# Kernel tuning notes

Measured on AMD Instinct MI355X. Metric: run time of the kernel, lower is better.

The kernel has to match this reference:

```python
import jax, jax.numpy as jnp
import numpy as np

D = 256      # d_model
H = 8        # n_heads
HD = D // H  # head_dim = 32
P = 16       # point dim per head


def setup_inputs() -> dict:
    key = jax.random.key(0)
    ks = jax.random.split(key, 12)
    B, S = 2, 2048
    w = lambda k, shape: jax.random.normal(k, shape, jnp.float32) * 0.02
    return {
        "seq_repr": jax.random.normal(ks[0], (B, S, D), jnp.float32),
        "coords": jax.random.normal(ks[1], (B, S, 3, 3), jnp.float32),
        "frames": jax.random.normal(ks[2], (B, S, 4), jnp.float32),
        "mask": jnp.ones((B, S), jnp.int32),
        "Wq": w(ks[3], (D, D)), "bq": jnp.zeros((D,), jnp.float32),
        "Wk": w(ks[4], (D, D)), "bk": jnp.zeros((D,), jnp.float32),
        "Wv": w(ks[5], (D, D)), "bv": jnp.zeros((D,), jnp.float32),
        "Wpq": w(ks[6], (3, H * P)), "bpq": jnp.zeros((H * P,), jnp.float32),
        "Wpk": w(ks[7], (3, H * P)), "bpk": jnp.zeros((H * P,), jnp.float32),
        "Wo": w(ks[8], (D, D)), "bo": jnp.zeros((D,), jnp.float32),
        "Wpo": w(ks[9], (H * P, 3)), "bpo": jnp.zeros((3,), jnp.float32),
        "attn_bias": jnp.zeros((H,), jnp.float32),
    }


def reference(seq_repr, coords, frames, mask, Wq, bq, Wk, bk, Wv, bv,
              Wpq, bpq, Wpk, bpk, Wo, bo, Wpo, bpo, attn_bias):
    B, S, _ = seq_repr.shape
    q = (seq_repr @ Wq + bq).reshape(B, S, H, HD)
    k = (seq_repr @ Wk + bk).reshape(B, S, H, HD)
    v = (seq_repr @ Wv + bv).reshape(B, S, H, HD)

    rep = coords[..., 1, :]                                  # [B,S,3] representative atom
    pq = (rep @ Wpq + bpq).reshape(B, S, H, P)
    pk = (rep @ Wpk + bpk).reshape(B, S, H, P)

    scale = 1.0 / np.sqrt(HD)
    scores = (jnp.einsum('bihd,bjhd->bhij', q, k) * scale
              + jnp.einsum('bihp,bjhp->bhij', pq, pk) * 0.25  # 1/sqrt(16)
              + attn_bias[None, :, None, None])

    mask2d = (mask[:, :, None] * mask[:, None, :])[:, None]  # [B,1,S,S]
    scores = jnp.where(mask2d == 0, jnp.float32(-1e9), scores)

    w = jax.nn.softmax(scores, axis=-1)                      # [B,H,S,S]

    seq_ctx = jnp.einsum('bhij,bjhd->bihd', w, v).reshape(B, S, D)
    pt_ctx = jnp.einsum('bhij,bjhp->bihp', w, pq).reshape(B, S, H * P)

    seq_out = seq_ctx @ Wo + bo                              # [B,S,D]
    point_out = pt_ctx @ Wpo + bpo                           # [B,S,3]
    return (seq_out, point_out)
```

## Files before the change

### kernel.cpp

```cpp
#include <hip/hip_runtime.h>
#include <hip/hip_bf16.h>

#define D_ 256
#define H_ 8
#define B_ 2
#define S_ 2048
#define MTOT 4096
#define AUGQ 64
#define NBH 16
#define KPAD 72
#define NSPLIT 4
#define NJ 8
#define LOG2E 1.4426950408889634f

typedef __attribute__((ext_vector_type(8))) short short8;
typedef __attribute__((ext_vector_type(4))) short short4v;
typedef __attribute__((ext_vector_type(4))) float f32x4;

static __device__ __forceinline__ short bf16_of(float f) {
  union { __hip_bfloat16 h; short s; } u;
  u.h = __float2bfloat16(f);
  return u.s;
}
static __device__ __forceinline__ float f_of_bf16(short s) {
  union { float f; unsigned int u; } u;
  u.u = ((unsigned int)(unsigned short)s) << 16;
  return u.f;
}

static __device__ __forceinline__ int sinv64(int c) {
  return (((((c >> 2) & 1) << 1) | ((c >> 5) & 1)) << 4) + (((c >> 3) & 3) << 2) + (c & 3);
}


__global__ __launch_bounds__(256) void prep_all(
    const float* __restrict__ Wq, const float* __restrict__ Wk,
    const float* __restrict__ Wv, const float* __restrict__ Wo,
    const float* __restrict__ X, const float* __restrict__ coords,
    const int* __restrict__ mask,
    const float* __restrict__ Wpq, const float* __restrict__ bpq,
    const float* __restrict__ Wpk, const float* __restrict__ bpk,
    short* __restrict__ Wqkv_t, short* __restrict__ Wo_t,
    short* __restrict__ Xb,
    short* __restrict__ Qa, short* __restrict__ Ka, short* __restrict__ VaT) {
  int bid = blockIdx.x, tid = threadIdx.x;

  if (bid < 64) {
    __shared__ short T[64][72];
    const float* src;
    short* dst;
    int k0, n0g;
    if (bid < 48) {
      int nt = bid >> 2;
      k0 = (bid & 3) * 64;
      n0g = nt * 64;
      src = (n0g < 256) ? Wq : (n0g < 512 ? Wk : Wv);
      dst = Wqkv_t;
    } else {
      int t2 = bid - 48;
      k0 = (t2 & 3) * 64;
      n0g = (t2 >> 2) * 64;
      src = Wo;
      dst = Wo_t;
    }
    int ncol = n0g & 255;
    int rr = tid >> 4, cc = (tid & 15) * 4;
#pragma unroll
    for (int i = 0; i < 4; i++) {
      int r = rr + i * 16;
      f32x4 v = *reinterpret_cast<const f32x4*>(&src[(size_t)(k0 + r) * 256 + ncol + cc]);
      T[cc + 0][r] = bf16_of(v[0]);
      T[cc + 1][r] = bf16_of(v[1]);
      T[cc + 2][r] = bf16_of(v[2]);
      T[cc + 3][r] = bf16_of(v[3]);
    }
    __syncthreads();
    int n = tid >> 2, kk = (tid & 3) * 16;
    *reinterpret_cast<short8*>(&dst[(size_t)(n0g + n) * 256 + k0 + kk]) =
        *reinterpret_cast<const short8*>(&T[n][kk]);
    *reinterpret_cast<short8*>(&dst[(size_t)(n0g + n) * 256 + k0 + kk + 8]) =
        *reinterpret_cast<const short8*>(&T[n][kk + 8]);
    return;
  }

  if (bid < 576) {
    size_t i = (size_t)(bid - 64) * 2048 + tid * 8;
    f32x4 v0 = *reinterpret_cast<const f32x4*>(&X[i]);
    f32x4 v1 = *reinterpret_cast<const f32x4*>(&X[i + 4]);
    short8 o;
    o[0] = bf16_of(v0[0]); o[1] = bf16_of(v0[1]); o[2] = bf16_of(v0[2]); o[3] = bf16_of(v0[3]);
    o[4] = bf16_of(v1[0]); o[5] = bf16_of(v1[1]); o[6] = bf16_of(v1[2]); o[7] = bf16_of(v1[3]);
    *reinterpret_cast<short8*>(&Xb[i]) = o;
    return;
  }

  if (bid < 704) {
    int idx = (bid - 576) * 256 + tid;
    int m = idx >> 3, h = idx & 7;
    int b = m >> 11, s = m & 2047;
    float r0 = coords[m * 9 + 3], r1 = coords[m * 9 + 4], r2 = coords[m * 9 + 5];
    size_t base = ((size_t)(b * 8 + h) * S_ + s) * AUGQ;
    short8 pqv[2], pkv[2];
#pragma unroll
    for (int c = 0; c < 2; c++)
#pragma unroll
      for (int i = 0; i < 8; i++) {
        int j = h * 16 + c * 8 + i;
        float pq = r0 * Wpq[j] + r1 * Wpq[128 + j] + r2 * Wpq[256 + j] + bpq[j];
        float pk = r0 * Wpk[j] + r1 * Wpk[128 + j] + r2 * Wpk[256 + j] + bpk[j];
        pqv[c][i] = bf16_of(pq * LOG2E);
        pkv[c][i] = bf16_of(pk * 0.25f);
      }
    short8 padq = {};
    padq[0] = bf16_of(LOG2E);
    short8 padk = {};
    padk[0] = mask[m] ? (short)0 : bf16_of(-1e9f);
    short8 z = {};
    *reinterpret_cast<short8*>(&Qa[base + 32]) = pqv[0];
    *reinterpret_cast<short8*>(&Qa[base + 40]) = pqv[1];
    *reinterpret_cast<short8*>(&Qa[base + 48]) = padq;
    *reinterpret_cast<short8*>(&Qa[base + 56]) = z;
    *reinterpret_cast<short8*>(&Ka[base + 32]) = pkv[0];
    *reinterpret_cast<short8*>(&Ka[base + 40]) = pkv[1];
    *reinterpret_cast<short8*>(&Ka[base + 48]) = padk;
    *reinterpret_cast<short8*>(&Ka[base + 56]) = z;
    return;
  }

  {
    int idx = (bid - 704) * 256 + tid;
    int s8 = idx & 255, p = (idx >> 8) & 15, bh = idx >> 12;
    int b = bh >> 3, h = bh & 7, j = h * 16 + p;
    float w0 = Wpq[j], w1 = Wpq[128 + j], w2 = Wpq[256 + j], bb = bpq[j];
    short8 o;
#pragma unroll
    for (int i = 0; i < 8; i++) {
      int c = (s8 & 7) * 8 + i;
      int m = b * 2048 + (s8 >> 3) * 64 + sinv64(c);
      o[i] = bf16_of(coords[m * 9 + 3] * w0 + coords[m * 9 + 4] * w1 +
                     coords[m * 9 + 5] * w2 + bb);
    }
    *reinterpret_cast<short8*>(&VaT[((size_t)bh * 48 + 32 + p) * S_ + s8 * 8]) = o;
  }
}


__global__ __launch_bounds__(256) void qkv_gemm(
    const short* __restrict__ Xb, const short* __restrict__ Wt,
    const float* __restrict__ bq, const float* __restrict__ bk, const float* __restrict__ bv,
    short* __restrict__ Qa, short* __restrict__ Ka, short* __restrict__ VaT) {
  __shared__ __align__(16) short As[64 * 136];
  __shared__ __align__(16) short Bs[64 * 136];
  int m0 = blockIdx.x * 64, n0 = blockIdx.y * 64;
  int tid = threadIdx.x, lane = tid & 63, w = tid >> 6;
  int t = lane & 15, g = lane >> 4, kf = g * 8;
  int wr = (w >> 1) * 32, wc = (w & 1) * 32;
  f32x4 acc[2][2] = {};
  int srow = tid >> 2, skc = (tid & 3) * 32;
  for (int ph = 0; ph < 2; ph++) {
    int k0 = ph * 128;
    __syncthreads();
    {
      const uint4* xsrc = reinterpret_cast<const uint4*>(&Xb[(size_t)(m0 + srow) * 256 + k0 + skc]);
      const uint4* wsrc = reinterpret_cast<const uint4*>(&Wt[(size_t)(n0 + srow) * 256 + k0 + skc]);
#pragma unroll
      for (int i = 0; i < 4; i++)
        *reinterpret_cast<uint4*>(&As[srow * 136 + skc + i * 8]) = xsrc[i];
#pragma unroll
      for (int i = 0; i < 4; i++)
        *reinterpret_cast<uint4*>(&Bs[srow * 136 + skc + i * 8]) = wsrc[i];
    }
    __syncthreads();
#pragma unroll
    for (int kk = 0; kk < 4; kk++) {
      short8 a[2], bb[2];
#pragma unroll
      for (int i = 0; i < 2; i++)
        a[i] = *reinterpret_cast<const short8*>(&As[(wr + i * 16 + t) * 136 + kk * 32 + kf]);
#pragma unroll
      for (int jj = 0; jj < 2; jj++)
        bb[jj] = *reinterpret_cast<const short8*>(&Bs[(wc + jj * 16 + t) * 136 + kk * 32 + kf]);
#pragma unroll
      for (int i = 0; i < 2; i++)
#pragma unroll
        for (int jj = 0; jj < 2; jj++)
          acc[i][jj] = __builtin_amdgcn_mfma_f32_16x16x32_bf16(a[i], bb[jj], acc[i][jj], 0, 0, 0);
    }
  }
  __syncthreads();
  short* Cs = As;
  const float scale = 0.17677669529663687f * LOG2E;
  int b = m0 >> 11, sbase = m0 & 2047;
#pragma unroll
  for (int i = 0; i < 2; i++)
#pragma unroll
    for (int jj = 0; jj < 2; jj++)
#pragma unroll
      for (int r = 0; r < 4; r++) {
        int rl = wr + i * 16 + g * 4 + r;
        int cl = wc + jj * 16 + t;
        int n = n0 + cl;
        float v = acc[i][jj][r];
        if (n < 256) v = (v + bq[n]) * scale;
        else if (n < 512) v = v + bk[n - 256];
        else v = v + bv[n - 512];
        Cs[rl * 72 + cl] = bf16_of(v);
      }
  __syncthreads();
  if (n0 < 512) {
#pragma unroll
    for (int i2 = 0; i2 < 2; i2++) {
      int task = tid + i2 * 256;
      int row = task >> 3, c = task & 7;
      int n = n0 + c * 8;
      short* dst = (n < 256) ? Qa : Ka;
      int nn = n & 255;
      int hh = nn >> 5, d = nn & 31;
      *reinterpret_cast<short8*>(&dst[((size_t)(b * 8 + hh) * S_ + sbase + row) * AUGQ + d]) =
          *reinterpret_cast<const short8*>(&Cs[row * 72 + c * 8]);
    }
  } else {
    int hv0 = (n0 - 512) >> 5;
#pragma unroll
    for (int i2 = 0; i2 < 2; i2++) {
      int task = tid + i2 * 256;
      int fl = task >> 3, s8 = task & 7;
      short8 o;
#pragma unroll
      for (int i = 0; i < 8; i++) o[i] = Cs[sinv64(s8 * 8 + i) * 72 + fl];
      int hh = hv0 + (fl >> 5), d = fl & 31;
      *reinterpret_cast<short8*>(&VaT[((size_t)(b * 8 + hh) * 48 + d) * S_ + sbase + s8 * 8]) = o;
    }
  }
}


__global__ __launch_bounds__(256, 4) void attn(
    const short* __restrict__ Qa, const short* __restrict__ Ka,
    const short* __restrict__ VaT,
    short* __restrict__ Ctx, float* __restrict__ AccL) {
  __shared__ __align__(16) char smem[32256];

  int bid = blockIdx.x;
  int xcd = bid & 7, slot = bid >> 3;
  int gidx = xcd * 8 + (slot >> 4);
  int it = slot & 15;
  int split = gidx & 3;
  int bhv = gidx >> 2;

  int tid = threadIdx.x, lane = tid & 63, w = tid >> 6;
  int t = lane & 15, g = lane >> 4, kf = g * 8;
  int q0w = it * 128 + w * 32;
  size_t bh = (size_t)bhv * S_;

  short8 aq[2][2];
#pragma unroll
  for (int g2 = 0; g2 < 2; g2++)
#pragma unroll
    for (int c = 0; c < 2; c++)
      aq[g2][c] = *reinterpret_cast<const short8*>(
          &Qa[(bh + q0w + g2 * 16 + t) * AUGQ + c * 32 + kf]);

  f32x4 OaccA[3] = {}, OaccB[3] = {};
  float lsum0 = 0.f, lsum1 = 0.f;

  uint4 kreg0, kreg1, vreg0, vreg1;
  int srow = tid >> 3, sko = (tid & 7) * 8;
  const int jt0 = split * NJ;

  auto issue = [&](int jt) {
    const uint4* ks = reinterpret_cast<const uint4*>(&Ka[(bh + jt * 64) * AUGQ]);
    kreg0 = ks[tid];
    kreg1 = ks[tid + 256];
    size_t vb = (size_t)bhv * 48 * S_ + jt * 64;
    vreg0 = *reinterpret_cast<const uint4*>(&VaT[vb + (size_t)srow * S_ + sko]);
    if (tid < 128)
      vreg1 = *reinterpret_cast<const uint4*>(&VaT[vb + (size_t)(srow + 32) * S_ + sko]);
  };
  auto commit = [&](int buf) {
    short* Kd = (short*)(smem + buf * 9216);
    short* Vd = (short*)(smem + 18432 + buf * 6912);
    *reinterpret_cast<uint4*>(&Kd[srow * KPAD + sko]) = kreg0;
    *reinterpret_cast<uint4*>(&Kd[(srow + 32) * KPAD + sko]) = kreg1;
    *reinterpret_cast<uint4*>(&Vd[srow * KPAD + sko]) = vreg0;
    if (tid < 128)
      *reinterpret_cast<uint4*>(&Vd[(srow + 32) * KPAD + sko]) = vreg1;
  };

  issue(jt0);
  commit(0);
  __syncthreads();

  for (int j = 0; j < NJ; j++) {
    int cur = j & 1;
    if (j + 1 < NJ) issue(jt0 + j + 1);
    const short* Kc = (const short*)(smem + cur * 9216);
    const short* Vc = (const short*)(smem + 18432 + cur * 6912);
    short8 pA[2], pB[2];
#pragma unroll
    for (int sub = 0; sub < 4; sub++) {
      short8 ka0 = *reinterpret_cast<const short8*>(&Kc[(sub * 16 + t) * KPAD + kf]);
      short8 ka1 = *reinterpret_cast<const short8*>(&Kc[(sub * 16 + t) * KPAD + 32 + kf]);
      f32x4 sA = {}, sB = {};
      sA = __builtin_amdgcn_mfma_f32_16x16x32_bf16(ka0, aq[0][0], sA, 0, 0, 0);
      sA = __builtin_amdgcn_mfma_f32_16x16x32_bf16(ka1, aq[0][1], sA, 0, 0, 0);
      sB = __builtin_amdgcn_mfma_f32_16x16x32_bf16(ka0, aq[1][0], sB, 0, 0, 0);
      sB = __builtin_amdgcn_mfma_f32_16x16x32_bf16(ka1, aq[1][1], sB, 0, 0, 0);
      float a0 = exp2f(sA[0]), a1 = exp2f(sA[1]), a2 = exp2f(sA[2]), a3 = exp2f(sA[3]);
      float b0 = exp2f(sB[0]), b1 = exp2f(sB[1]), b2 = exp2f(sB[2]), b3 = exp2f(sB[3]);
      lsum0 += (a0 + a1) + (a2 + a3);
      lsum1 += (b0 + b1) + (b2 + b3);
      int ww = sub & 1, off = (sub >> 1) * 4;
      pA[ww][off + 0] = bf16_of(a0); pA[ww][off + 1] = bf16_of(a1);
      pA[ww][off + 2] = bf16_of(a2); pA[ww][off + 3] = bf16_of(a3);
      pB[ww][off + 0] = bf16_of(b0); pB[ww][off + 1] = bf16_of(b1);
      pB[ww][off + 2] = bf16_of(b2); pB[ww][off + 3] = bf16_of(b3);
    }
    __builtin_amdgcn_s_setprio(1);
#pragma unroll
    for (int tt = 0; tt < 3; tt++) {
#pragma unroll
      for (int w2 = 0; w2 < 2; w2++) {
        short8 va = *reinterpret_cast<const short8*>(&Vc[(tt * 16 + t) * KPAD + w2 * 32 + kf]);
        OaccA[tt] = __builtin_amdgcn_mfma_f32_16x16x32_bf16(va, pA[w2], OaccA[tt], 0, 0, 0);
        OaccB[tt] = __builtin_amdgcn_mfma_f32_16x16x32_bf16(va, pB[w2], OaccB[tt], 0, 0, 0);
      }
    }
    __builtin_amdgcn_s_setprio(0);
    if (j + 1 < NJ) commit(cur ^ 1);
    __syncthreads();
  }

  lsum0 += __shfl_xor(lsum0, 16); lsum0 += __shfl_xor(lsum0, 32);
  lsum1 += __shfl_xor(lsum1, 16); lsum1 += __shfl_xor(lsum1, 32);

  float* Of = (float*)smem;
#pragma unroll
  for (int tt = 0; tt < 3; tt++)
#pragma unroll
    for (int r = 0; r < 4; r++) {
      Of[(w * 32 + t) * 52 + tt * 16 + g * 4 + r] = OaccA[tt][r];
      Of[(w * 32 + 16 + t) * 52 + tt * 16 + g * 4 + r] = OaccB[tt][r];
    }
  if (lane < 16) {
    size_t lb = (size_t)(split * NBH + bhv) * S_ + q0w + lane;
    AccL[lb] = lsum0;
    AccL[lb + 16] = lsum1;
  }
  __syncthreads();
  short* CtxP = Ctx + (size_t)split * NBH * S_ * 48;
  size_t obase = bh + it * 128;
  for (int task = tid; task < 768; task += 256) {
    int row = task / 6, c8 = task % 6;
    const float* src = &Of[row * 52 + c8 * 8];
    short8 o;
#pragma unroll
    for (int i = 0; i < 8; i++) o[i] = bf16_of(src[i]);
    *reinterpret_cast<short8*>(&CtxP[(obase + row) * 48 + c8 * 8]) = o;
  }
}


__global__ __launch_bounds__(512) void out_gemm(
    const short* __restrict__ Ctx, const float* __restrict__ AccL,
    const short* __restrict__ Wot, const float* __restrict__ bo,
    const float* __restrict__ Wpo, const float* __restrict__ bpo,
    float* __restrict__ Out) {
  const size_t CTXSZ = (size_t)NBH * S_ * 48;
  int m0 = blockIdx.x * 64;
  int tid = threadIdx.x;
  int b = m0 >> 11, sbase = m0 & 2047;

  if (blockIdx.y == 4) {
    int row = tid >> 3, hh = tid & 7;
    int m = m0 + row, s = sbase + row;
    size_t rowO = (size_t)(b * 8 + hh) * S_ + s;
    float l = 0.f;
#pragma unroll
    for (int sp = 0; sp < NSPLIT; sp++) l += AccL[(size_t)sp * NBH * S_ + rowO];
    float inv = 1.0f / l;
    float a0 = 0.f, a1 = 0.f, a2 = 0.f;
#pragma unroll
    for (int half = 0; half < 2; half++) {
      float sum[8] = {};
#pragma unroll
      for (int sp = 0; sp < NSPLIT; sp++) {
        short8 v = *reinterpret_cast<const short8*>(&Ctx[sp * CTXSZ + rowO * 48 + 32 + half * 8]);
#pragma unroll
        for (int c = 0; c < 8; c++) sum[c] += f_of_bf16(v[c]);
      }
#pragma unroll
      for (int c = 0; c < 8; c++) {
        float val = sum[c] * inv;
        int j = hh * 16 + half * 8 + c;
        a0 += val * Wpo[j * 3 + 0];
        a1 += val * Wpo[j * 3 + 1];
        a2 += val * Wpo[j * 3 + 2];
      }
    }
    a0 += __shfl_xor(a0, 1); a0 += __shfl_xor(a0, 2); a0 += __shfl_xor(a0, 4);
    a1 += __shfl_xor(a1, 1); a1 += __shfl_xor(a1, 2); a1 += __shfl_xor(a1, 4);
    a2 += __shfl_xor(a2, 1); a2 += __shfl_xor(a2, 2); a2 += __shfl_xor(a2, 4);
    if (hh == 0) {
      float* po = Out + (size_t)MTOT * 256;
      po[(size_t)m * 3 + 0] = a0 + bpo[0];
      po[(size_t)m * 3 + 1] = a1 + bpo[1];
      po[(size_t)m * 3 + 2] = a2 + bpo[2];
    }
    return;
  }

  __shared__ __align__(16) short As[64 * 136];
  __shared__ __align__(16) short Bs[64 * 136];
  int n0 = blockIdx.y * 64;
  int lane = tid & 63, w = tid >> 6;
  int t = lane & 15, g = lane >> 4, kf = g * 8;
  int wm = w & 3, wn = w >> 2;
  f32x4 acc[2] = {};
  int srow = tid >> 3, skc = (tid & 7) * 16;
  for (int ph = 0; ph < 2; ph++) {
    int k0 = ph * 128;
    __syncthreads();
    {
      int kg = k0 + skc;
      int hh = kg >> 5, d0 = kg & 31;
      size_t rowO = (size_t)(b * 8 + hh) * S_ + sbase + srow;
      float l = 0.f;
#pragma unroll
      for (int sp = 0; sp < NSPLIT; sp++) l += AccL[(size_t)sp * NBH * S_ + rowO];
      float inv = 1.0f / l;
#pragma unroll
      for (int half = 0; half < 2; half++) {
        float sum[8] = {};
#pragma unroll
        for (int sp = 0; sp < NSPLIT; sp++) {
          short8 a = *reinterpret_cast<const short8*>(&Ctx[sp * CTXSZ + rowO * 48 + d0 + half * 8]);
#pragma unroll
          for (int c = 0; c < 8; c++) sum[c] += f_of_bf16(a[c]);
        }
        short8 o;
#pragma unroll
        for (int c = 0; c < 8; c++) o[c] = bf16_of(sum[c] * inv);
        *reinterpret_cast<short8*>(&As[srow * 136 + skc + half * 8]) = o;
      }
      *reinterpret_cast<uint4*>(&Bs[srow * 136 + skc]) =
          *reinterpret_cast<const uint4*>(&Wot[(size_t)(n0 + srow) * 256 + kg]);
      *reinterpret_cast<uint4*>(&Bs[srow * 136 + skc + 8]) =
          *reinterpret_cast<const uint4*>(&Wot[(size_t)(n0 + srow) * 256 + kg + 8]);
    }
    __syncthreads();
#pragma unroll
    for (int kk = 0; kk < 4; kk++) {
      short8 a = *reinterpret_cast<const short8*>(&As[(wm * 16 + t) * 136 + kk * 32 + kf]);
#pragma unroll
      for (int jj = 0; jj < 2; jj++) {
        short8 bb = *reinterpret_cast<const short8*>(&Bs[(wn * 32 + jj * 16 + t) * 136 + kk * 32 + kf]);
        acc[jj] = __builtin_amdgcn_mfma_f32_16x16x32_bf16(a, bb, acc[jj], 0, 0, 0);
      }
    }
  }
#pragma unroll
  for (int jj = 0; jj < 2; jj++)
#pragma unroll
    for (int r = 0; r < 4; r++) {
      int mrow = m0 + wm * 16 + g * 4 + r;
      int n = n0 + wn * 32 + jj * 16 + t;
      Out[(size_t)mrow * 256 + n] = acc[jj][r] + bo[n];
    }
}


extern "C" void kernel_launch(void* const* d_in, const int* in_sizes, int n_in,
                              void* d_out, int out_size, void* d_ws, size_t ws_size,
                              hipStream_t stream) {
  const float* seq    = (const float*)d_in[0];
  const float* coords = (const float*)d_in[1];
  const int*   mask   = (const int*)d_in[3];
  const float* Wq  = (const float*)d_in[4];
  const float* bq  = (const float*)d_in[5];
  const float* Wk  = (const float*)d_in[6];
  const float* bk  = (const float*)d_in[7];
  const float* Wv  = (const float*)d_in[8];
  const float* bv  = (const float*)d_in[9];
  const float* Wpq = (const float*)d_in[10];
  const float* bpq = (const float*)d_in[11];
  const float* Wpk = (const float*)d_in[12];
  const float* bpk = (const float*)d_in[13];
  const float* Wo  = (const float*)d_in[14];
  const float* bo  = (const float*)d_in[15];
  const float* Wpo = (const float*)d_in[16];
  const float* bpo = (const float*)d_in[17];
  float* out = (float*)d_out;

  char* ws = (char*)d_ws;
  short* Wqkv_t = (short*)ws; ws += 768 * 256 * 2;
  short* Wo_t   = (short*)ws; ws += 256 * 256 * 2;
  short* Xb     = (short*)ws; ws += (size_t)MTOT * D_ * 2;
  short* Qa     = (short*)ws; ws += (size_t)NBH * S_ * AUGQ * 2;
  short* Ka     = (short*)ws; ws += (size_t)NBH * S_ * AUGQ * 2;
  short* VaT    = (short*)ws; ws += (size_t)NBH * 48 * S_ * 2;
  short* Ctx    = (short*)ws; ws += (size_t)NSPLIT * NBH * S_ * 48 * 2;
  float* AccL   = (float*)ws; ws += (size_t)NSPLIT * NBH * S_ * 4;

  prep_all<<<960, 256, 0, stream>>>(Wq, Wk, Wv, Wo, seq, coords, mask,
                                    Wpq, bpq, Wpk, bpk,
                                    Wqkv_t, Wo_t, Xb, Qa, Ka, VaT);
  qkv_gemm<<<dim3(64, 12), 256, 0, stream>>>(Xb, Wqkv_t, bq, bk, bv, Qa, Ka, VaT);
  attn<<<1024, 256, 0, stream>>>(Qa, Ka, VaT, Ctx, AccL);
  out_gemm<<<dim3(64, 5), 512, 0, stream>>>(Ctx, AccL, Wo_t, bo, Wpo, bpo, out);
}
```

Baseline: 60.21 us.

## Load K/V tiles directly from global into registers, drop LDS double-buffering

The attention kernel stops staging K and V tiles through double-buffered shared memory with per-iteration barriers. Each wave now loads its K and V MFMA operands straight from global memory (relying on L1/L2) into registers, and the loop no longer synchronises. exp2f is also swapped for the hardware exp2 builtin. The risk is that the four waves now each fetch the same K/V data, raising global and L2 traffic, and the latency of those loads may no longer be hidden by the software prefetch.

```diff
diff --git a/kernel.cpp b/kernel.cpp
--- a/kernel.cpp
+++ b/kernel.cpp
@@ -8,7 +8,6 @@
 #define MTOT 4096
 #define AUGQ 64
 #define NBH 16
-#define KPAD 72
 #define NSPLIT 4
 #define NJ 8
 #define LOG2E 1.4426950408889634f
@@ -26,6 +25,13 @@
   union { float f; unsigned int u; } u;
   u.u = ((unsigned int)(unsigned short)s) << 16;
   return u.f;
+}
+static __device__ __forceinline__ float fast_exp2(float x) {
+#if defined(__has_builtin) && __has_builtin(__builtin_amdgcn_exp2f)
+  return __builtin_amdgcn_exp2f(x);
+#else
+  return exp2f(x);
+#endif
 }
 
 static __device__ __forceinline__ int sinv64(int c) {
@@ -239,7 +245,7 @@
     const short* __restrict__ Qa, const short* __restrict__ Ka,
     const short* __restrict__ VaT,
     short* __restrict__ Ctx, float* __restrict__ AccL) {
-  __shared__ __align__(16) char smem[32256];
+  __shared__ __align__(16) float Of[128 * 52];
 
   int bid = blockIdx.x;
   int xcd = bid & 7, slot = bid >> 3;
@@ -263,51 +269,39 @@
 
   f32x4 OaccA[3] = {}, OaccB[3] = {};
   float lsum0 = 0.f, lsum1 = 0.f;
-
-  uint4 kreg0, kreg1, vreg0, vreg1;
-  int srow = tid >> 3, sko = (tid & 7) * 8;
   const int jt0 = split * NJ;
-
-  auto issue = [&](int jt) {
-    const uint4* ks = reinterpret_cast<const uint4*>(&Ka[(bh + jt * 64) * AUGQ]);
-    kreg0 = ks[tid];
-    kreg1 = ks[tid + 256];
-    size_t vb = (size_t)bhv * 48 * S_ + jt * 64;
-    vreg0 = *reinterpret_cast<const uint4*>(&VaT[vb + (size_t)srow * S_ + sko]);
-    if (tid < 128)
-      vreg1 = *reinterpret_cast<const uint4*>(&VaT[vb + (size_t)(srow + 32) * S_ + sko]);
-  };
-  auto commit = [&](int buf) {
-    short* Kd = (short*)(smem + buf * 9216);
-    short* Vd = (short*)(smem + 18432 + buf * 6912);
-    *reinterpret_cast<uint4*>(&Kd[srow * KPAD + sko]) = kreg0;
-    *reinterpret_cast<uint4*>(&Kd[(srow + 32) * KPAD + sko]) = kreg1;
-    *reinterpret_cast<uint4*>(&Vd[srow * KPAD + sko]) = vreg0;
-    if (tid < 128)
-      *reinterpret_cast<uint4*>(&Vd[(srow + 32) * KPAD + sko]) = vreg1;
-  };
-
-  issue(jt0);
-  commit(0);
-  __syncthreads();
+  const short* Kbh = &Ka[bh * AUGQ];
+  const short* Vbh = &VaT[(size_t)bhv * 48 * S_];
 
   for (int j = 0; j < NJ; j++) {
-    int cur = j & 1;
-    if (j + 1 < NJ) issue(jt0 + j + 1);
-    const short* Kc = (const short*)(smem + cur * 9216);
-    const short* Vc = (const short*)(smem + 18432 + cur * 6912);
+    int jt = jt0 + j;
+    const short* kt = &Kbh[(size_t)(jt * 64) * AUGQ];
+    const short* vt = &Vbh[jt * 64];
+    short8 ka0[4], ka1[4], va[3][2];
+#pragma unroll
+    for (int sub = 0; sub < 4; sub++) {
+      ka0[sub] = *reinterpret_cast<const short8*>(&kt[(sub * 16 + t) * AUGQ + kf]);
+      ka1[sub] = *reinterpret_cast<const short8*>(&kt[(sub * 16 + t) * AUGQ + 32 + kf]);
+    }
+#pragma unroll
+    for (int tt = 0; tt < 3; tt++)
+#pragma unroll
+      for (int w2 = 0; w2 < 2; w2++)
+        va[tt][w2] = *reinterpret_cast<const short8*>(
+            &vt[(size_t)(tt * 16 + t) * S_ + w2 * 32 + kf]);
+
     short8 pA[2], pB[2];
 #pragma unroll
     for (int sub = 0; sub < 4; sub++) {
-      short8 ka0 = *reinterpret_cast<const short8*>(&Kc[(sub * 16 + t) * KPAD + kf]);
-      short8 ka1 = *reinterpret_cast<const short8*>(&Kc[(sub * 16 + t) * KPAD + 32 + kf]);
       f32x4 sA = {}, sB = {};
-      sA = __builtin_amdgcn_mfma_f32_16x16x32_bf16(ka0, aq[0][0], sA, 0, 0, 0);
-      sA = __builtin_amdgcn_mfma_f32_16x16x32_bf16(ka1, aq[0][1], sA, 0, 0, 0);
-      sB = __builtin_amdgcn_mfma_f32_16x16x32_bf16(ka0, aq[1][0], sB, 0, 0, 0);
-      sB = __builtin_amdgcn_mfma_f32_16x16x32_bf16(ka1, aq[1][1], sB, 0, 0, 0);
-      float a0 = exp2f(sA[0]), a1 = exp2f(sA[1]), a2 = exp2f(sA[2]), a3 = exp2f(sA[3]);
-      float b0 = exp2f(sB[0]), b1 = exp2f(sB[1]), b2 = exp2f(sB[2]), b3 = exp2f(sB[3]);
+      sA = __builtin_amdgcn_mfma_f32_16x16x32_bf16(ka0[sub], aq[0][0], sA, 0, 0, 0);
+      sA = __builtin_amdgcn_mfma_f32_16x16x32_bf16(ka1[sub], aq[0][1], sA, 0, 0, 0);
+      sB = __builtin_amdgcn_mfma_f32_16x16x32_bf16(ka0[sub], aq[1][0], sB, 0, 0, 0);
+      sB = __builtin_amdgcn_mfma_f32_16x16x32_bf16(ka1[sub], aq[1][1], sB, 0, 0, 0);
+      float a0 = fast_exp2(sA[0]), a1 = fast_exp2(sA[1]);
+      float a2 = fast_exp2(sA[2]), a3 = fast_exp2(sA[3]);
+      float b0 = fast_exp2(sB[0]), b1 = fast_exp2(sB[1]);
+      float b2 = fast_exp2(sB[2]), b3 = fast_exp2(sB[3]);
       lsum0 += (a0 + a1) + (a2 + a3);
       lsum1 += (b0 + b1) + (b2 + b3);
       int ww = sub & 1, off = (sub >> 1) * 4;
@@ -321,20 +315,16 @@
     for (int tt = 0; tt < 3; tt++) {
 #pragma unroll
       for (int w2 = 0; w2 < 2; w2++) {
-        short8 va = *reinterpret_cast<const short8*>(&Vc[(tt * 16 + t) * KPAD + w2 * 32 + kf]);
-        OaccA[tt] = __builtin_amdgcn_mfma_f32_16x16x32_bf16(va, pA[w2], OaccA[tt], 0, 0, 0);
-        OaccB[tt] = __builtin_amdgcn_mfma_f32_16x16x32_bf16(va, pB[w2], OaccB[tt], 0, 0, 0);
+        OaccA[tt] = __builtin_amdgcn_mfma_f32_16x16x32_bf16(va[tt][w2], pA[w2], OaccA[tt], 0, 0, 0);
+        OaccB[tt] = __builtin_amdgcn_mfma_f32_16x16x32_bf16(va[tt][w2], pB[w2], OaccB[tt], 0, 0, 0);
       }
     }
     __builtin_amdgcn_s_setprio(0);
-    if (j + 1 < NJ) commit(cur ^ 1);
-    __syncthreads();
   }
 
   lsum0 += __shfl_xor(lsum0, 16); lsum0 += __shfl_xor(lsum0, 32);
   lsum1 += __shfl_xor(lsum1, 16); lsum1 += __shfl_xor(lsum1, 32);
 
-  float* Of = (float*)smem;
 #pragma unroll
   for (int tt = 0; tt < 3; tt++)
 #pragma unroll
```

After: 88.26 us. 1.47x slower.

## Enlarge QKV GEMM tiles to 128x128 with register-staged K loop

Applied to the files above, without the earlier changes.

The QKV projection GEMM now uses 128x128 output tiles per block, with each wave computing a 64x64 sub-tile as a 4x4 grid of MFMAs, and steps through K in 64-wide chunks. Global loads for each chunk are first staged in registers and then written to shared memory. The intent is more operand reuse per byte loaded and fewer blocks. The trade-off is that the grid drops from 768 to 192 blocks, which is below one block per CU on a 256-CU part, and each thread needs more accumulator registers.

```diff
diff --git a/kernel.cpp b/kernel.cpp
--- a/kernel.cpp
+++ b/kernel.cpp
@@ -149,87 +149,95 @@
     const short* __restrict__ Xb, const short* __restrict__ Wt,
     const float* __restrict__ bq, const float* __restrict__ bk, const float* __restrict__ bv,
     short* __restrict__ Qa, short* __restrict__ Ka, short* __restrict__ VaT) {
-  __shared__ __align__(16) short As[64 * 136];
-  __shared__ __align__(16) short Bs[64 * 136];
-  int m0 = blockIdx.x * 64, n0 = blockIdx.y * 64;
+  __shared__ __align__(16) char smem[36864];
+  short* As = (short*)smem;
+  short* Bs = (short*)(smem + 18432);
+  int m0 = blockIdx.x * 128, n0 = blockIdx.y * 128;
   int tid = threadIdx.x, lane = tid & 63, w = tid >> 6;
   int t = lane & 15, g = lane >> 4, kf = g * 8;
-  int wr = (w >> 1) * 32, wc = (w & 1) * 32;
-  f32x4 acc[2][2] = {};
-  int srow = tid >> 2, skc = (tid & 3) * 32;
-  for (int ph = 0; ph < 2; ph++) {
-    int k0 = ph * 128;
+  int wr = (w >> 1) * 64, wc = (w & 1) * 64;
+  f32x4 acc[4][4] = {};
+  int srow = tid >> 1, shalf = (tid & 1) * 32;
+  for (int k0 = 0; k0 < 256; k0 += 64) {
+    uint4 aR[4], bR[4];
+    {
+      const uint4* ga = reinterpret_cast<const uint4*>(&Xb[(size_t)(m0 + srow) * 256 + k0 + shalf]);
+      const uint4* gb = reinterpret_cast<const uint4*>(&Wt[(size_t)(n0 + srow) * 256 + k0 + shalf]);
+#pragma unroll
+      for (int i = 0; i < 4; i++) aR[i] = ga[i];
+#pragma unroll
+      for (int i = 0; i < 4; i++) bR[i] = gb[i];
+    }
     __syncthreads();
-    {
-      const uint4* xsrc = reinterpret_cast<const uint4*>(&Xb[(size_t)(m0 + srow) * 256 + k0 + skc]);
-      const uint4* wsrc = reinterpret_cast<const uint4*>(&Wt[(size_t)(n0 + srow) * 256 + k0 + skc]);
+#pragma unroll
+    for (int i = 0; i < 4; i++)
+      *reinterpret_cast<uint4*>(&As[srow * 72 + shalf + i * 8]) = aR[i];
+#pragma unroll
+    for (int i = 0; i < 4; i++)
+      *reinterpret_cast<uint4*>(&Bs[srow * 72 + shalf + i * 8]) = bR[i];
+    __syncthreads();
+#pragma unroll
+    for (int kk = 0; kk < 2; kk++) {
+      short8 a[4], bb[4];
 #pragma unroll
       for (int i = 0; i < 4; i++)
-        *reinterpret_cast<uint4*>(&As[srow * 136 + skc + i * 8]) = xsrc[i];
+        a[i] = *reinterpret_cast<const short8*>(&As[(wr + i * 16 + t) * 72 + kk * 32 + kf]);
+#pragma unroll
+      for (int j = 0; j < 4; j++)
+        bb[j] = *reinterpret_cast<const short8*>(&Bs[(wc + j * 16 + t) * 72 + kk * 32 + kf]);
 #pragma unroll
       for (int i = 0; i < 4; i++)
-        *reinterpret_cast<uint4*>(&Bs[srow * 136 + skc + i * 8]) = wsrc[i];
-    }
-    __syncthreads();
-#pragma unroll
-    for (int kk = 0; kk < 4; kk++) {
-      short8 a[2], bb[2];
-#pragma unroll
-      for (int i = 0; i < 2; i++)
-        a[i] = *reinterpret_cast<const short8*>(&As[(wr + i * 16 + t) * 136 + kk * 32 + kf]);
-#pragma unroll
-      for (int jj = 0; jj < 2; jj++)
-        bb[jj] = *reinterpret_cast<const short8*>(&Bs[(wc + jj * 16 + t) * 136 + kk * 32 + kf]);
-#pragma unroll
-      for (int i = 0; i < 2; i++)
-#pragma unroll
-        for (int jj = 0; jj < 2; jj++)
-          acc[i][jj] = __builtin_amdgcn_mfma_f32_16x16x32_bf16(a[i], bb[jj], acc[i][jj], 0, 0, 0);
+#pragma unroll
+        for (int j = 0; j < 4; j++)
+          acc[i][j] = __builtin_amdgcn_mfma_f32_16x16x32_bf16(a[i], bb[j], acc[i][j], 0, 0, 0);
     }
   }
   __syncthreads();
-  short* Cs = As;
+  short* Cs = (short*)smem;
   const float scale = 0.17677669529663687f * LOG2E;
   int b = m0 >> 11, sbase = m0 & 2047;
 #pragma unroll
-  for (int i = 0; i < 2; i++)
-#pragma unroll
-    for (int jj = 0; jj < 2; jj++)
+  for (int i = 0; i < 4; i++)
+#pragma unroll
+    for (int j = 0; j < 4; j++)
 #pragma unroll
       for (int r = 0; r < 4; r++) {
         int rl = wr + i * 16 + g * 4 + r;
-        int cl = wc + jj * 16 + t;
+        int cl = wc + j * 16 + t;
         int n = n0 + cl;
-        float v = acc[i][jj][r];
+        float v = acc[i][j][r];
         if (n < 256) v = (v + bq[n]) * scale;
         else if (n < 512) v = v + bk[n - 256];
         else v = v + bv[n - 512];
-        Cs[rl * 72 + cl] = bf16_of(v);
+        Cs[rl * 136 + cl] = bf16_of(v);
       }
   __syncthreads();
   if (n0 < 512) {
 #pragma unroll
-    for (int i2 = 0; i2 < 2; i2++) {
+    for (int i2 = 0; i2 < 8; i2++) {
       int task = tid + i2 * 256;
-      int row = task >> 3, c = task & 7;
+      int row = task >> 4, c = task & 15;
       int n = n0 + c * 8;
       short* dst = (n < 256) ? Qa : Ka;
       int nn = n & 255;
       int hh = nn >> 5, d = nn & 31;
       *reinterpret_cast<short8*>(&dst[((size_t)(b * 8 + hh) * S_ + sbase + row) * AUGQ + d]) =
-          *reinterpret_cast<const short8*>(&Cs[row * 72 + c * 8]);
+          *reinterpret_cast<const short8*>(&Cs[row * 136 + c * 8]);
     }
   } else {
     int hv0 = (n0 - 512) >> 5;
 #pragma unroll
-    for (int i2 = 0; i2 < 2; i2++) {
+    for (int i2 = 0; i2 < 8; i2++) {
       int task = tid + i2 * 256;
-      int fl = task >> 3, s8 = task & 7;
+      int fl = task >> 4, sc = task & 15;
+      int h64 = sc >> 3, c8 = sc & 7;
       short8 o;
 #pragma unroll
-      for (int i = 0; i < 8; i++) o[i] = Cs[sinv64(s8 * 8 + i) * 72 + fl];
+      for (int i = 0; i < 8; i++)
+        o[i] = Cs[(h64 * 64 + sinv64(c8 * 8 + i)) * 136 + fl];
       int hh = hv0 + (fl >> 5), d = fl & 31;
-      *reinterpret_cast<short8*>(&VaT[((size_t)(b * 8 + hh) * 48 + d) * S_ + sbase + s8 * 8]) = o;
+      *reinterpret_cast<short8*>(
+          &VaT[((size_t)(b * 8 + hh) * 48 + d) * S_ + sbase + h64 * 64 + c8 * 8]) = o;
     }
   }
 }
@@ -505,7 +513,7 @@
   prep_all<<<960, 256, 0, stream>>>(Wq, Wk, Wv, Wo, seq, coords, mask,
                                     Wpq, bpq, Wpk, bpk,
                                     Wqkv_t, Wo_t, Xb, Qa, Ka, VaT);
-  qkv_gemm<<<dim3(64, 12), 256, 0, stream>>>(Xb, Wqkv_t, bq, bk, bv, Qa, Ka, VaT);
+  qkv_gemm<<<dim3(32, 6), 256, 0, stream>>>(Xb, Wqkv_t, bq, bk, bv, Qa, Ka, VaT);
   attn<<<1024, 256, 0, stream>>>(Qa, Ka, VaT, Ctx, AccL);
   out_gemm<<<dim3(64, 5), 512, 0, stream>>>(Ctx, AccL, Wo_t, bo, Wpo, bpo, out);
 }
```

New measurement: 74.83 us. 1.24x slower.
